# Optimization experiments

Hardware: AMD Instinct MI355X
Metric: run time of the kernel (lower is better)

Reference implementation:

```python
import jax, jax.numpy as jnp
import numpy as np

N_BINS = 15


def setup_inputs() -> dict:
    key = jax.random.key(0)
    k1, k2 = jax.random.split(key)
    N, C = 16777216, 3
    logits = jax.random.normal(k1, (N, C), dtype=jnp.float32)
    labels = jax.random.randint(k2, (N,), 0, C, dtype=jnp.int64)
    return {"logits": logits, "labels": labels}


def reference(logits, labels):
    # softmax + max over classes
    probs = jax.nn.softmax(logits, axis=1)
    confidences = jnp.max(probs, axis=1)            # [N]
    predictions = jnp.argmax(probs, axis=1)         # [N]
    accuracies = (predictions == labels).astype(logits.dtype)

    n = confidences.shape[0]
    # bin i covers (i/n_bins, (i+1)/n_bins]; first upper >= conf via side='left'
    uppers = jnp.linspace(0.0, 1.0, N_BINS + 1, dtype=logits.dtype)[1:]
    bin_idx = jnp.clip(jnp.searchsorted(uppers, confidences, side="left"), 0, N_BINS - 1)

    ones = jnp.ones_like(confidences)
    cnt = jax.ops.segment_sum(ones, bin_idx, num_segments=N_BINS)
    conf_sum = jax.ops.segment_sum(confidences, bin_idx, num_segments=N_BINS)
    acc_sum = jax.ops.segment_sum(accuracies, bin_idx, num_segments=N_BINS)

    safe_cnt = jnp.maximum(cnt, 1.0)
    gap = jnp.abs(conf_sum / safe_cnt - acc_sum / safe_cnt)
    prop = cnt / n
    ece = jnp.sum(jnp.where(cnt > 0, gap * prop, 0.0))
    return ece[None]  # shape (1,) like the torch module
```

## Files before the change

kernel.cpp:

```cpp
#include <hip/hip_runtime.h>
#include <math.h>

#define NBINS 15
#define THREADS 256
#define GRID 2048
#define BIN_LO 4
#define NACC (NBINS - BIN_LO)

__device__ __forceinline__ void process_row(float l0, float l1, float l2, int lab,
                                            float* a) {
  float m  = fmaxf(fmaxf(l0, l1), l2);
  float md = __builtin_amdgcn_fmed3f(l0, l1, l2);
  float mn = fminf(fminf(l0, l1), l2);
  float s  = 1.0f + __expf(md - m) + __expf(mn - m);
  float conf = __builtin_amdgcn_rcpf(s);
  float lm = (lab == 1) ? l1 : ((lab == 2) ? l2 : l0);
  float val = conf - ((lm >= m) ? 1.0f : 0.0f);
  int bin = (int)ceilf(conf * 15.0f) - 1;
  bin = bin < BIN_LO ? BIN_LO : (bin > NBINS - 1 ? NBINS - 1 : bin);
#pragma unroll
  for (int b = BIN_LO; b < NBINS; ++b) a[b - BIN_LO] += (bin == b) ? val : 0.0f;
}

__global__ __launch_bounds__(THREADS, 8) void ece_main(
    const float4* __restrict__ logits4, const int4* __restrict__ labels4,
    float* __restrict__ partial, int n) {
  float a[NACC];
#pragma unroll
  for (int i = 0; i < NACC; ++i) a[i] = 0.0f;

  const int nquads = n >> 2;
  const int total = gridDim.x * blockDim.x;
  const int iters = nquads / total;
  int q = blockIdx.x * blockDim.x + threadIdx.x;
#pragma unroll 2
  for (int it = 0; it < iters; ++it, q += total) {
    const float4* p = logits4 + 3 * (size_t)q;
    float4 x = p[0], y = p[1], z = p[2];
    int4 lb = labels4[q];
    process_row(x.x, x.y, x.z, lb.x, a);
    process_row(x.w, y.x, y.y, lb.y, a);
    process_row(y.z, y.w, z.x, lb.z, a);
    process_row(z.y, z.z, z.w, lb.w, a);
  }
  if (q < nquads) {
    const float4* p = logits4 + 3 * (size_t)q;
    float4 x = p[0], y = p[1], z = p[2];
    int4 lb = labels4[q];
    process_row(x.x, x.y, x.z, lb.x, a);
    process_row(x.w, y.x, y.y, lb.y, a);
    process_row(y.z, y.w, z.x, lb.z, a);
    process_row(z.y, z.z, z.w, lb.w, a);
  }

#pragma unroll
  for (int i = 0; i < NACC; ++i) {
    float v = a[i];
#pragma unroll
    for (int off = 32; off > 0; off >>= 1) v += __shfl_down(v, off, 64);
    a[i] = v;
  }
  __shared__ float s_part[THREADS / 64][NACC];
  const int wave = threadIdx.x >> 6;
  const int lane = threadIdx.x & 63;
  if (lane == 0) {
#pragma unroll
    for (int i = 0; i < NACC; ++i) s_part[wave][i] = a[i];
  }
  __syncthreads();
  if (threadIdx.x < NACC) {
    float v = 0.0f;
#pragma unroll
    for (int w = 0; w < THREADS / 64; ++w) v += s_part[w][threadIdx.x];
    partial[(size_t)threadIdx.x * gridDim.x + blockIdx.x] = v;
  }
}

__global__ __launch_bounds__(1024) void ece_final(
    const float* __restrict__ partial, const float* __restrict__ logits,
    const int* __restrict__ labels, float* __restrict__ out, int n, int nblocks) {
  __shared__ double sbin[NACC];
  const int wave = threadIdx.x >> 6;
  const int lane = threadIdx.x & 63;
  if (wave < NACC) {
    double v = 0.0;
    for (int i = lane; i < nblocks; i += 64)
      v += (double)partial[(size_t)wave * nblocks + i];
#pragma unroll
    for (int off = 32; off > 0; off >>= 1) v += __shfl_down(v, off, 64);
    if (lane == 0) sbin[wave] = v;
  }
  __syncthreads();
  if (threadIdx.x == 0) {
    float t[NACC];
#pragma unroll
    for (int i = 0; i < NACC; ++i) t[i] = 0.0f;
    for (int r = (n >> 2) << 2; r < n; ++r)
      process_row(logits[3 * r], logits[3 * r + 1], logits[3 * r + 2], labels[r], t);
    double ece = 0.0;
#pragma unroll
    for (int b = 0; b < NACC; ++b) ece += fabs(sbin[b] + (double)t[b]);
    out[0] = (float)(ece / (double)n);
  }
}

extern "C" void kernel_launch(void* const* d_in, const int* in_sizes, int n_in,
                              void* d_out, int out_size, void* d_ws, size_t ws_size,
                              hipStream_t stream) {
  const float4* logits4 = (const float4*)d_in[0];
  const int4* labels4 = (const int4*)d_in[1];
  const int n = in_sizes[1];
  float* partial = (float*)d_ws;
  ece_main<<<GRID, THREADS, 0, stream>>>(logits4, labels4, partial, n);
  ece_final<<<1, 1024, 0, stream>>>(partial, (const float*)d_in[0],
                                    (const int*)d_in[1], (float*)d_out, n, GRID);
}
```

Before: 57.97 us.

## Fuse final reduction into main kernel via double atomics and last-block counter

Replaces the second reduction kernel with per-block double-precision atomicAdds into 11 bin accumulators and a completion counter; the last block to finish computes the ECE and writes the output. This removes one kernel launch and the partial-array pass, but adds a memset per call and contention from 2048 blocks doing atomics on the same few addresses. Memory ordering relies on an s_waitcnt before the counter increment and relaxed atomic loads.

```diff
diff --git a/kernel.cpp b/kernel.cpp
--- a/kernel.cpp
+++ b/kernel.cpp
@@ -6,6 +6,7 @@
 #define GRID 2048
 #define BIN_LO 4
 #define NACC (NBINS - BIN_LO)
+
 
 __device__ __forceinline__ void process_row(float l0, float l1, float l2, int lab,
                                             float* a) {
@@ -24,7 +25,8 @@
 
 __global__ __launch_bounds__(THREADS, 8) void ece_main(
     const float4* __restrict__ logits4, const int4* __restrict__ labels4,
-    float* __restrict__ partial, int n) {
+    double* __restrict__ wsd, unsigned int* __restrict__ ctr,
+    float* __restrict__ out, int n) {
   float a[NACC];
 #pragma unroll
   for (int i = 0; i < NACC; ++i) a[i] = 0.0f;
@@ -68,38 +70,45 @@
     for (int i = 0; i < NACC; ++i) s_part[wave][i] = a[i];
   }
   __syncthreads();
-  if (threadIdx.x < NACC) {
+  if (wave != 0) return;
+
+  if (lane < NACC) {
     float v = 0.0f;
 #pragma unroll
-    for (int w = 0; w < THREADS / 64; ++w) v += s_part[w][threadIdx.x];
-    partial[(size_t)threadIdx.x * gridDim.x + blockIdx.x] = v;
+    for (int w = 0; w < THREADS / 64; ++w) v += s_part[w][lane];
+    atomicAdd(&wsd[lane], (double)v);
   }
-}
+  asm volatile("s_waitcnt vmcnt(0)" ::: "memory");
+  unsigned int old = 0;
+  if (lane == 0) old = atomicAdd(ctr, 1u);
+  old = __shfl(old, 0, 64);
+  if (old != (unsigned int)(gridDim.x - 1)) return;
 
-__global__ __launch_bounds__(1024) void ece_final(
-    const float* __restrict__ partial, const float* __restrict__ logits,
-    const int* __restrict__ labels, float* __restrict__ out, int n, int nblocks) {
-  __shared__ double sbin[NACC];
-  const int wave = threadIdx.x >> 6;
-  const int lane = threadIdx.x & 63;
-  if (wave < NACC) {
-    double v = 0.0;
-    for (int i = lane; i < nblocks; i += 64)
-      v += (double)partial[(size_t)wave * nblocks + i];
+  if (lane == 0) {
+    double ece = 0.0;
+    const int tail_lo = (n >> 2) << 2;
+    if (tail_lo == n) {
 #pragma unroll
-    for (int off = 32; off > 0; off >>= 1) v += __shfl_down(v, off, 64);
-    if (lane == 0) sbin[wave] = v;
-  }
-  __syncthreads();
-  if (threadIdx.x == 0) {
-    float t[NACC];
+      for (int b = 0; b < NACC; ++b) {
+        double d = __hip_atomic_load(&wsd[b], __ATOMIC_RELAXED,
+                                     __HIP_MEMORY_SCOPE_AGENT);
+        ece += fabs(d);
+      }
+    } else {
+      float t[NACC];
 #pragma unroll
-    for (int i = 0; i < NACC; ++i) t[i] = 0.0f;
-    for (int r = (n >> 2) << 2; r < n; ++r)
-      process_row(logits[3 * r], logits[3 * r + 1], logits[3 * r + 2], labels[r], t);
-    double ece = 0.0;
+      for (int i = 0; i < NACC; ++i) t[i] = 0.0f;
+      const float* lf = (const float*)logits4;
+      const int* li = (const int*)labels4;
+      for (int r = tail_lo; r < n; ++r)
+        process_row(lf[3 * r], lf[3 * r + 1], lf[3 * r + 2], li[r], t);
 #pragma unroll
-    for (int b = 0; b < NACC; ++b) ece += fabs(sbin[b] + (double)t[b]);
+      for (int b = 0; b < NACC; ++b) {
+        double d = __hip_atomic_load(&wsd[b], __ATOMIC_RELAXED,
+                                     __HIP_MEMORY_SCOPE_AGENT);
+        ece += fabs(d + (double)t[b]);
+      }
+    }
     out[0] = (float)(ece / (double)n);
   }
 }
@@ -110,8 +119,9 @@
   const float4* logits4 = (const float4*)d_in[0];
   const int4* labels4 = (const int4*)d_in[1];
   const int n = in_sizes[1];
-  float* partial = (float*)d_ws;
-  ece_main<<<GRID, THREADS, 0, stream>>>(logits4, labels4, partial, n);
-  ece_final<<<1, 1024, 0, stream>>>(partial, (const float*)d_in[0],
-                                    (const int*)d_in[1], (float*)d_out, n, GRID);
+  double* wsd = (double*)d_ws;
+  unsigned int* ctr = (unsigned int*)((char*)d_ws + NACC * sizeof(double));
+  hipMemsetAsync(d_ws, 0, 96, stream);
+  ece_main<<<GRID, THREADS, 0, stream>>>(logits4, labels4, wsd, ctr,
+                                         (float*)d_out, n);
 }
```

New measurement: 78.28 us. +35.0%, slower.
